# Optimization experiments

Measured on AMD Instinct MI355X. Metric: run time of the kernel, lower is better.

## Reference

```python
import jax, jax.numpy as jnp
import numpy as np

B, S, IN, H, OUT, L = 256, 512, 27, 128, 7, 10


def setup_inputs() -> dict:
    key = jax.random.key(0)
    ks = jax.random.split(key, 12)
    sc = 0.05
    return {
        "x": jax.random.normal(ks[0], (B, S, IN), dtype=jnp.float32),
        # layer 0 input projection (input_size != hidden), PyTorch gate order i,f,g,o
        "w_ih0": jax.random.normal(ks[1], (4 * H, IN), dtype=jnp.float32) * sc,
        # layers 1..9 input projections
        "w_ih": jax.random.normal(ks[2], (L - 1, 4 * H, H), dtype=jnp.float32) * sc,
        "w_hh": jax.random.normal(ks[3], (L, 4 * H, H), dtype=jnp.float32) * sc,
        "b_ih": jax.random.normal(ks[4], (L, 4 * H), dtype=jnp.float32) * sc,
        "b_hh": jax.random.normal(ks[5], (L, 4 * H), dtype=jnp.float32) * sc,
        "attn_w": jax.random.normal(ks[6], (H, H), dtype=jnp.float32) * sc,
        "attn_b": jax.random.normal(ks[7], (H,), dtype=jnp.float32) * sc,
        "v_w": jax.random.normal(ks[8], (1, H), dtype=jnp.float32) * sc,
        "v_b": jax.random.normal(ks[9], (1,), dtype=jnp.float32) * sc,
        "fc_w": jax.random.normal(ks[10], (OUT, H), dtype=jnp.float32) * sc,
        "fc_b": jax.random.normal(ks[11], (OUT,), dtype=jnp.float32) * sc,
    }


def _lstm_layer(x_seq, w_ih, w_hh, b_ih, b_hh):
    # x_seq: [B, S, D_in] -> hidden sequence [B, S, H]
    b, s, _ = x_seq.shape
    h_dim = w_hh.shape[1]
    # precompute input-gate GEMM for the whole sequence (big matmul)
    xg = jnp.einsum('bsd,gd->bsg', x_seq, w_ih) + b_ih + b_hh  # [B, S, 4H]

    def step(carry, xg_t):
        h, c = carry
        gates = xg_t + h @ w_hh.T  # [B, 4H]
        i, f, g, o = jnp.split(gates, 4, axis=-1)
        i = jax.nn.sigmoid(i)
        f = jax.nn.sigmoid(f)
        g = jnp.tanh(g)
        o = jax.nn.sigmoid(o)
        c = f * c + i * g
        h = o * jnp.tanh(c)
        return (h, c), h

    init = (jnp.zeros((b, h_dim), x_seq.dtype), jnp.zeros((b, h_dim), x_seq.dtype))
    _, hs = jax.lax.scan(step, init, jnp.swapaxes(xg, 0, 1))  # [S, B, H]
    return jnp.swapaxes(hs, 0, 1)


def reference(x, w_ih0, w_ih, w_hh, b_ih, b_hh, attn_w, attn_b, v_w, v_b, fc_w, fc_b):
    # 10-layer stacked LSTM (dropout inactive at inference)
    out = _lstm_layer(x, w_ih0, w_hh[0], b_ih[0], b_hh[0])
    for l in range(1, L):
        out = _lstm_layer(out, w_ih[l - 1], w_hh[l], b_ih[l], b_hh[l])
    # additive attention pooling
    scores = jnp.tanh(out @ attn_w.T + attn_b)            # [B, S, H]
    logits = scores @ v_w.T + v_b                          # [B, S, 1]
    weights = jax.nn.softmax(logits, axis=1)               # softmax over time
    context = jnp.sum(weights * out, axis=1)               # [B, H]
    return context @ fc_w.T + fc_b                         # [B, OUT]
```

## Files before the change

### kernel.cpp

```cpp
#include <hip/hip_runtime.h>
#include <cstdint>
#include <cstddef>

#define S_LEN 512
#define HDIM  128
#define G4    512
#define BATCH 256
#define NLAYER 10
#define ROWS  16
#define NBLK  (BATCH / ROWS)
#define RING  10

typedef float f32x4 __attribute__((ext_vector_type(4)));
typedef short short8 __attribute__((ext_vector_type(8)));
typedef _Float16 h16x4 __attribute__((ext_vector_type(4)));
typedef _Float16 h16x8 __attribute__((ext_vector_type(8)));

__device__ __forceinline__ float fsig(float x) {
  return __builtin_amdgcn_rcpf(1.0f + __expf(-x));
}
__device__ __forceinline__ float ftanh(float x) {
  return fmaf(2.0f, __builtin_amdgcn_rcpf(1.0f + __expf(-2.0f * x)), -1.0f);
}
__device__ __forceinline__ unsigned short bf16_rne(float x) {
  unsigned int u = __float_as_uint(x);
  unsigned int r = (u + 0x7fffu + ((u >> 16) & 1u)) >> 16;
  return (unsigned short)r;
}
__device__ __forceinline__ float bf16_to_f(unsigned short h) {
  return __uint_as_float(((unsigned int)h) << 16);
}


__global__ void split_w(const float* __restrict__ W, unsigned short* __restrict__ hi,
                        unsigned short* __restrict__ lo, int n)
{
  int i = blockIdx.x * 256 + threadIdx.x;
  if (i < n) {
    float x = W[i];
    unsigned short h = bf16_rne(x);
    hi[i] = h;
    lo[i] = bf16_rne(x - bf16_to_f(h));
  }
}

__global__ void w0_prep(const float* __restrict__ W, unsigned short* __restrict__ hi,
                        unsigned short* __restrict__ lo)
{
  int i = blockIdx.x * 256 + threadIdx.x;
  if (i >= 512 * 32) return;
  int col = i >> 5, k = i & 31;
  float v = (k < 27) ? W[col * 27 + k] : 0.f;
  unsigned short h = bf16_rne(v);
  hi[i] = h;
  lo[i] = bf16_rne(v - bf16_to_f(h));
}

__global__ __launch_bounds__(256)
void whh_prep(const float* __restrict__ Whh, unsigned short* __restrict__ WF)
{
  int idx = blockIdx.x * 256 + threadIdx.x;
  if (idx >= NLAYER * 16 * 16 * 64) return;
  int ln = idx & 63;
  int f  = (idx >> 6) & 15;
  int w  = (idx >> 10) & 15;
  int l  = idx >> 14;
  int ct = f >> 3, ks = (f >> 1) & 3, hl = f & 1;
  int col = w * 32 + ct * 16 + (ln & 15);
  int k0  = ks * 32 + (ln >> 4) * 8;
  const float* src = Whh + ((size_t)l * G4 + col) * HDIM + k0;
  unsigned short out[8];
  #pragma unroll
  for (int j = 0; j < 8; ++j) {
    float x = src[j];
    unsigned short h = bf16_rne(x);
    out[j] = hl ? bf16_rne(x - bf16_to_f(h)) : h;
  }
  *(short8*)&WF[(size_t)idx * 8] = *(short8*)out;
}

__global__ __launch_bounds__(1024, 4)
void gemm_st(const float* __restrict__ x,
             const float* __restrict__ H0, const float* __restrict__ H1,
             const unsigned short* __restrict__ W0hi, const unsigned short* __restrict__ W0lo,
             const unsigned short* __restrict__ WhiAll, const unsigned short* __restrict__ WloAll,
             const float* __restrict__ bihAll, const float* __restrict__ bhhAll,
             _Float16* __restrict__ XGring, int tchShift, int s, int lmin)
{
  __shared__ unsigned short Ahi[4 * 16 * HDIM];
  __shared__ unsigned short Bhi[64 * HDIM];
  __shared__ unsigned short Blo[64 * HDIM];

  const int l  = lmin + blockIdx.z;
  const int c  = s - l;
  const int bi = blockIdx.x;
  const int tg = blockIdx.y;
  const int tid = threadIdx.x;
  const int t0 = c << tchShift;
  const size_t slotF = ((size_t)BATCH * G4) << tchShift;
  _Float16* __restrict__ XG = XGring + (size_t)(c % RING) * slotF;
  const float* bih = bihAll + l * G4;
  const float* bhh = bhhAll + l * G4;

  {
    int row = tid >> 4;
    int tw = row >> 4, rr = row & 15;
    int ks16 = tid & 15;
    int b = bi * 16 + rr;
    int t = t0 + tg * 4 + tw;
    if (l == 0) {
      if (ks16 < 4) {
        int kg = ks16 * 8;
        const float* ap = &x[((size_t)b * S_LEN + t) * 27];
        unsigned short h8[8];
        #pragma unroll
        for (int j = 0; j < 8; ++j) {
          int k = kg + j;
          float v = (k < 27) ? ap[k] : 0.f;
          h8[j] = bf16_rne(v);
        }
        int byA = tw * 4096 + ((rr * 256 + kg * 2) ^ ((rr & 7) << 4));
        *(short8*)((char*)Ahi + byA) = *(short8*)h8;
      }
    } else {
      int kg = ks16 * 8;
      const float* Asrc = ((l - 1) & 1) ? H1 : H0;
      const float* ap = &Asrc[((size_t)b * S_LEN + t) * HDIM + kg];
      float4 v0 = *(const float4*)ap;
      float4 v1 = *(const float4*)(ap + 4);
      float xs[8] = {v0.x, v0.y, v0.z, v0.w, v1.x, v1.y, v1.z, v1.w};
      unsigned short h8[8];
      #pragma unroll
      for (int j = 0; j < 8; ++j) h8[j] = bf16_rne(xs[j]);
      int byA = tw * 4096 + ((rr * 256 + kg * 2) ^ ((rr & 7) << 4));
      *(short8*)((char*)Ahi + byA) = *(short8*)h8;
    }
  }
  __syncthreads();

  const int ln = tid & 63, lr = ln & 15, lk = ln >> 4;
  const int w16 = tid >> 6;
  const int tw = w16 & 3, cg = w16 >> 2;
  const int tt = tg * 4 + tw;
  const unsigned short* Whi = WhiAll + (size_t)(l - 1) * G4 * HDIM;
  const unsigned short* Wlo = WloAll + (size_t)(l - 1) * G4 * HDIM;

  short8 ah[4];
  #pragma unroll
  for (int ks = 0; ks < 4; ++ks) {
    int fo = (lr * 256 + ks * 64 + lk * 16) ^ ((lr & 7) << 4);
    ah[ks] = *(const short8*)((char*)Ahi + tw * 4096 + fo);
  }
  #pragma unroll
  for (int ks = 0; ks < 4; ++ks) asm("" : "+v"(ah[ks]));

  for (int by = 0; by < 8; ++by) {
    if (l == 0) {
      if (tid < 256) {
        int cc = tid >> 2, kg = (tid & 3) * 8;
        int col = by * 64 + cc;
        int byB = (cc * 256 + kg * 2) ^ ((cc & 7) << 4);
        *(short8*)((char*)Bhi + byB) = *(const short8*)&W0hi[(size_t)col * 32 + kg];
        *(short8*)((char*)Blo + byB) = *(const short8*)&W0lo[(size_t)col * 32 + kg];
      }
    } else {
      int cc = tid >> 4, kg = (tid & 15) * 8;
      int col = by * 64 + cc;
      int byB = (cc * 256 + kg * 2) ^ ((cc & 7) << 4);
      *(short8*)((char*)Bhi + byB) = *(const short8*)&Whi[(size_t)col * HDIM + kg];
      *(short8*)((char*)Blo + byB) = *(const short8*)&Wlo[(size_t)col * HDIM + kg];
    }
    __syncthreads();

    f32x4 acc = {0.f, 0.f, 0.f, 0.f};
    if (l == 0) {
      int fo = (lr * 256 + lk * 16) ^ ((lr & 7) << 4);
      short8 bh = *(const short8*)((char*)Bhi + cg * 4096 + fo);
      short8 bl = *(const short8*)((char*)Blo + cg * 4096 + fo);
      acc = __builtin_amdgcn_mfma_f32_16x16x32_bf16(ah[0], bh, acc, 0, 0, 0);
      acc = __builtin_amdgcn_mfma_f32_16x16x32_bf16(ah[0], bl, acc, 0, 0, 0);
    } else {
      #pragma unroll
      for (int ks = 0; ks < 4; ++ks) {
        int fo = (lr * 256 + ks * 64 + lk * 16) ^ ((lr & 7) << 4);
        short8 bh = *(const short8*)((char*)Bhi + cg * 4096 + fo);
        short8 bl = *(const short8*)((char*)Blo + cg * 4096 + fo);
        acc = __builtin_amdgcn_mfma_f32_16x16x32_bf16(ah[ks], bh, acc, 0, 0, 0);
        acc = __builtin_amdgcn_mfma_f32_16x16x32_bf16(ah[ks], bl, acc, 0, 0, 0);
      }
    }
    int col = by * 64 + cg * 16 + lr;
    float bs = bih[col] + bhh[col];
    h16x4 o;
    #pragma unroll
    for (int j = 0; j < 4; ++j) o[j] = (_Float16)(acc[j] + bs);
    size_t base = ((((size_t)tt * 16 + bi) * 16) + by * 2 + (cg >> 1)) << 9;
    *(h16x4*)(XG + base + ln * 8 + (cg & 1) * 4) = o;
    __syncthreads();
  }
}

__global__ __launch_bounds__(1024, 4)
void scan_mfma(const _Float16* __restrict__ XGring, int tchShift,
               const unsigned short* __restrict__ WF,
               float* __restrict__ H0, float* __restrict__ H1,
               float* __restrict__ cstAll, int s, int lmin)
{
  const int l  = lmin + blockIdx.y;
  const int ch = s - l;
  const int TCHr = 1 << tchShift;
  const int t0 = ch << tchShift;
  const _Float16* __restrict__ XG =
      XGring + (size_t)(ch % RING) * (((size_t)BATCH * G4) << tchShift);
  float* __restrict__ Hout = (l & 1) ? H1 : H0;
  float* __restrict__ cst  = cstAll + (size_t)l * BATCH * HDIM;
  const int B0  = blockIdx.x * ROWS;
  const int tid = threadIdx.x;
  const int w   = tid >> 6;
  const int ln  = tid & 63;
  const int lr  = ln & 15;
  const int lk  = ln >> 4;

  __shared__ unsigned short hA[ROWS * HDIM];
  __shared__ float pp[ROWS * G4];

  short8 bf[16];
  {
    const unsigned short* wfp = WF + (((size_t)l * 16 + w) * 16) * 512 + (size_t)ln * 8;
    #pragma unroll
    for (int f = 0; f < 16; ++f) bf[f] = *(const short8*)(wfp + (size_t)f * 512);
    #pragma unroll
    for (int f = 0; f < 16; ++f) asm("" : "+v"(bf[f]));
  }

  const int grow0 = tid >> 7;
  const int grow1 = grow0 + 8;
  const int ghid  = tid & 127;
  float c0 = 0.f, c1 = 0.f;
  {
    float h0v = 0.f, h1v = 0.f;
    if (t0 > 0) {
      h0v = Hout[((size_t)(B0 + grow0) * S_LEN + (t0 - 1)) * HDIM + ghid];
      h1v = Hout[((size_t)(B0 + grow1) * S_LEN + (t0 - 1)) * HDIM + ghid];
      c0 = cst[(B0 + grow0) * HDIM + ghid];
      c1 = cst[(B0 + grow1) * HDIM + ghid];
    }
    int by0 = (grow0 * 256 + ghid * 2) ^ ((grow0 & 7) << 4);
    int by1 = (grow1 * 256 + ghid * 2) ^ ((grow1 & 7) << 4);
    *(unsigned short*)((char*)hA + by0) = bf16_rne(h0v);
    *(unsigned short*)((char*)hA + by1) = bf16_rne(h1v);
  }
  __syncthreads();

  const _Float16* xgp = XG + (((size_t)blockIdx.x * 16 + w) << 9) + (ln << 3);
  float* hout0 = Hout + ((size_t)(B0 + grow0) * S_LEN + t0) * HDIM + ghid;
  float* hout1 = Hout + ((size_t)(B0 + grow1) * S_LEN + t0) * HDIM + ghid;

  h16x8 xg_c = *(const h16x8*)xgp;

  for (int tt = 0; tt < TCHr; ++tt) {
    const h16x8 xgh = xg_c;
    const _Float16* xgn = xgp + (size_t)BATCH * G4;
    if (tt + 1 < TCHr) xg_c = *(const h16x8*)xgn;

    f32x4 acc0 = {0.f, 0.f, 0.f, 0.f}, acc1 = {0.f, 0.f, 0.f, 0.f};
    #pragma unroll
    for (int ks = 0; ks < 4; ++ks) {
      const int by = (lr * 256 + ks * 64 + lk * 16) ^ ((lr & 7) << 4);
      short8 ah = *(const short8*)((const char*)hA + by);
      acc0 = __builtin_amdgcn_mfma_f32_16x16x32_bf16(ah, bf[(ks << 1) | 0], acc0, 0, 0, 0);
      acc0 = __builtin_amdgcn_mfma_f32_16x16x32_bf16(ah, bf[(ks << 1) | 1], acc0, 0, 0, 0);
      acc1 = __builtin_amdgcn_mfma_f32_16x16x32_bf16(ah, bf[8 | (ks << 1) | 0], acc1, 0, 0, 0);
      acc1 = __builtin_amdgcn_mfma_f32_16x16x32_bf16(ah, bf[8 | (ks << 1) | 1], acc1, 0, 0, 0);
    }

    #pragma unroll
    for (int j = 0; j < 4; ++j) {
      int r16 = lk * 4 + j;
      int colA = w * 32 + lr;
      int byA = (r16 * 2048 + colA * 4) ^ ((r16 & 3) << 5);
      *(float*)((char*)pp + byA) = acc0[j] + (float)xgh[j];
      int colB = colA + 16;
      int byB = (r16 * 2048 + colB * 4) ^ ((r16 & 3) << 5);
      *(float*)((char*)pp + byB) = acc1[j] + (float)xgh[4 + j];
    }
    __syncthreads();

    {
      int b0 = grow0 * 2048, x0 = (grow0 & 3) << 5;
      float pi = *(const float*)((const char*)pp + ((b0 + (ghid)       * 4) ^ x0));
      float pf = *(const float*)((const char*)pp + ((b0 + (128 + ghid) * 4) ^ x0));
      float pg = *(const float*)((const char*)pp + ((b0 + (256 + ghid) * 4) ^ x0));
      float po = *(const float*)((const char*)pp + ((b0 + (384 + ghid) * 4) ^ x0));
      float gi = fsig(pi), gf = fsig(pf), gg = ftanh(pg), go = fsig(po);
      c0 = fmaf(gf, c0, gi * gg);
      float h0 = go * ftanh(c0);

      int b1 = grow1 * 2048, x1 = (grow1 & 3) << 5;
      float qi = *(const float*)((const char*)pp + ((b1 + (ghid)       * 4) ^ x1));
      float qf = *(const float*)((const char*)pp + ((b1 + (128 + ghid) * 4) ^ x1));
      float qg = *(const float*)((const char*)pp + ((b1 + (256 + ghid) * 4) ^ x1));
      float qo = *(const float*)((const char*)pp + ((b1 + (384 + ghid) * 4) ^ x1));
      float hi_ = fsig(qi), hf = fsig(qf), hg = ftanh(qg), ho = fsig(qo);
      c1 = fmaf(hf, c1, hi_ * hg);
      float h1 = ho * ftanh(c1);

      hout0[0] = h0;
      hout1[0] = h1;
      int by0 = (grow0 * 256 + ghid * 2) ^ ((grow0 & 7) << 4);
      int by1 = (grow1 * 256 + ghid * 2) ^ ((grow1 & 7) << 4);
      *(unsigned short*)((char*)hA + by0) = bf16_rne(h0);
      *(unsigned short*)((char*)hA + by1) = bf16_rne(h1);
    }
    __syncthreads();
    xgp = xgn;
    hout0 += HDIM;
    hout1 += HDIM;
  }
  cst[(B0 + grow0) * HDIM + ghid] = c0;
  cst[(B0 + grow1) * HDIM + ghid] = c1;
}

__global__ __launch_bounds__(256, 2)
void attn1_mfma(const float* __restrict__ Hs,
                const unsigned short* __restrict__ AWhi,
                const unsigned short* __restrict__ AWlo,
                const float* __restrict__ attn_b, const float* __restrict__ v_w,
                const float* __restrict__ v_b, float* __restrict__ logits)
{
  __shared__ unsigned short Ahi[64][136];
  __shared__ unsigned short Alo[64][136];
  __shared__ unsigned short Bhi[128][72];
  __shared__ unsigned short Blo[128][72];
  const int tid = threadIdx.x;
  const int rowBase = blockIdx.x * 64;

  #pragma unroll
  for (int it = 0; it < 4; ++it) {
    int idx = tid + it * 256;
    int rr  = idx >> 4;
    int kg  = (idx & 15) * 8;
    const float* ap = &Hs[(size_t)(rowBase + rr) * HDIM + kg];
    float4 v0 = *(const float4*)ap;
    float4 v1 = *(const float4*)(ap + 4);
    float xs[8] = {v0.x, v0.y, v0.z, v0.w, v1.x, v1.y, v1.z, v1.w};
    unsigned short h[8], l8[8];
    #pragma unroll
    for (int j = 0; j < 8; ++j) {
      h[j]  = bf16_rne(xs[j]);
      l8[j] = bf16_rne(xs[j] - bf16_to_f(h[j]));
    }
    *(short8*)&Ahi[rr][kg] = *(short8*)h;
    *(short8*)&Alo[rr][kg] = *(short8*)l8;
  }

  const int w    = tid >> 6;
  const int ln   = tid & 63;
  const int fr   = ln & 15;
  const int kgrp = (ln >> 4) * 8;

  f32x4 acc[8] = {};
  #pragma unroll
  for (int kh = 0; kh < 2; ++kh) {
    __syncthreads();
    #pragma unroll
    for (int it = 0; it < 4; ++it) {
      int idx = tid + it * 256;
      int cc  = idx >> 3;
      int kg  = (idx & 7) * 8;
      *(short8*)&Bhi[cc][kg] = *(const short8*)&AWhi[(size_t)cc * HDIM + kh * 64 + kg];
      *(short8*)&Blo[cc][kg] = *(const short8*)&AWlo[(size_t)cc * HDIM + kh * 64 + kg];
    }
    __syncthreads();
    #pragma unroll
    for (int ks = 0; ks < 2; ++ks) {
      const int k0 = kh * 64 + ks * 32 + kgrp;
      const int kb = ks * 32 + kgrp;
      short8 ah = *(const short8*)&Ahi[(w << 4) + fr][k0];
      short8 al = *(const short8*)&Alo[(w << 4) + fr][k0];
      #pragma unroll
      for (int nt = 0; nt < 8; ++nt) {
        short8 bh = *(const short8*)&Bhi[nt * 16 + fr][kb];
        short8 bl = *(const short8*)&Blo[nt * 16 + fr][kb];
        acc[nt] = __builtin_amdgcn_mfma_f32_16x16x32_bf16(ah, bh, acc[nt], 0, 0, 0);
        acc[nt] = __builtin_amdgcn_mfma_f32_16x16x32_bf16(ah, bl, acc[nt], 0, 0, 0);
        acc[nt] = __builtin_amdgcn_mfma_f32_16x16x32_bf16(al, bh, acc[nt], 0, 0, 0);
      }
    }
  }

  float parts[4] = {0.f, 0.f, 0.f, 0.f};
  #pragma unroll
  for (int nt = 0; nt < 8; ++nt) {
    const int col = nt * 16 + fr;
    const float ab = attn_b[col];
    const float vw = v_w[col];
    #pragma unroll
    for (int j = 0; j < 4; ++j)
      parts[j] = fmaf(ftanh(acc[nt][j] + ab), vw, parts[j]);
  }
  #pragma unroll
  for (int j = 0; j < 4; ++j) {
    #pragma unroll
    for (int off = 1; off < 16; off <<= 1)
      parts[j] += __shfl_xor(parts[j], off);
  }
  if (fr == 0) {
    const float vb = v_b[0];
    #pragma unroll
    for (int j = 0; j < 4; ++j)
      logits[rowBase + (w << 4) + ((ln >> 4) << 2) + j] = parts[j] + vb;
  }
}

__global__ __launch_bounds__(128)
void attn2(const float* __restrict__ Hs, const float* __restrict__ logits,
           const float* __restrict__ fc_w, const float* __restrict__ fc_b,
           float* __restrict__ outp)
{
  const int b   = blockIdx.x;
  const int tid = threadIdx.x;
  __shared__ float pbuf[S_LEN];
  __shared__ float red[4];
  __shared__ float ctx_s[HDIM];
  float l0 = logits[b * S_LEN + tid];
  float l1 = logits[b * S_LEN + 128 + tid];
  float l2 = logits[b * S_LEN + 256 + tid];
  float l3 = logits[b * S_LEN + 384 + tid];
  float m = fmaxf(fmaxf(l0, l1), fmaxf(l2, l3));
  #pragma unroll
  for (int off = 1; off < 64; off <<= 1) m = fmaxf(m, __shfl_xor(m, off));
  if ((tid & 63) == 0) red[tid >> 6] = m;
  __syncthreads();
  m = fmaxf(red[0], red[1]);
  float p0 = __expf(l0 - m), p1 = __expf(l1 - m), p2 = __expf(l2 - m), p3 = __expf(l3 - m);
  pbuf[tid] = p0; pbuf[tid + 128] = p1; pbuf[tid + 256] = p2; pbuf[tid + 384] = p3;
  float sum = (p0 + p1) + (p2 + p3);
  #pragma unroll
  for (int off = 1; off < 64; off <<= 1) sum += __shfl_xor(sum, off);
  if ((tid & 63) == 0) red[2 + (tid >> 6)] = sum;
  __syncthreads();
  const float sinv = 1.0f / (red[2] + red[3]);
  float acc = 0.f;
  const float* hp = Hs + (size_t)b * S_LEN * HDIM + tid;
  #pragma unroll 4
  for (int t = 0; t < S_LEN; ++t) acc = fmaf(pbuf[t], hp[(size_t)t * HDIM], acc);
  ctx_s[tid] = acc * sinv;
  __syncthreads();
  if (tid < 7) {
    float a = fc_b[tid];
    const float* fw = fc_w + tid * HDIM;
    #pragma unroll 8
    for (int k = 0; k < HDIM; ++k) a = fmaf(ctx_s[k], fw[k], a);
    outp[b * 7 + tid] = a;
  }
}

extern "C" void kernel_launch(void* const* d_in, const int* in_sizes, int n_in,
                              void* d_out, int out_size, void* d_ws, size_t ws_size,
                              hipStream_t stream)
{
  const float* x      = (const float*)d_in[0];
  const float* w_ih0  = (const float*)d_in[1];
  const float* w_ih   = (const float*)d_in[2];
  const float* w_hh   = (const float*)d_in[3];
  const float* b_ih   = (const float*)d_in[4];
  const float* b_hh   = (const float*)d_in[5];
  const float* attn_w = (const float*)d_in[6];
  const float* attn_b = (const float*)d_in[7];
  const float* v_w    = (const float*)d_in[8];
  const float* v_b    = (const float*)d_in[9];
  const float* fc_w   = (const float*)d_in[10];
  const float* fc_b   = (const float*)d_in[11];
  float* outp = (float*)d_out;

  const size_t szH_b  = (size_t)BATCH * S_LEN * HDIM * 4;
  const int    nWih   = (NLAYER - 1) * G4 * HDIM;
  const size_t nWF    = (size_t)NLAYER * 16 * 16 * 64 * 8;
  const int    nAW    = HDIM * HDIM;
  const int    nW0    = 512 * 32;
  const size_t fixed  = 2 * szH_b + (size_t)NLAYER * BATCH * HDIM * 4
                      + (size_t)nWih * 2 * 2 + nWF * 2 + (size_t)nAW * 2 * 2
                      + (size_t)nW0 * 2 * 2
                      + (size_t)BATCH * S_LEN * 4;

  int tchShift = -1;
  for (int sh = 6; sh >= 3; --sh) {
    size_t ringBytes = (size_t)RING * (((size_t)BATCH * G4) << sh) * 2;
    if (ws_size >= fixed + ringBytes) { tchShift = sh; break; }
  }
  if (tchShift < 0) return;
  const int TCHr = 1 << tchShift;
  const int NCHr = S_LEN >> tchShift;

  char* p = (char*)d_ws;
  _Float16* XGring = (_Float16*)p;
  p += (size_t)RING * (((size_t)BATCH * G4) << tchShift) * 2;
  float* H0  = (float*)p; p += szH_b;
  float* H1  = (float*)p; p += szH_b;
  float* cst = (float*)p; p += (size_t)NLAYER * BATCH * HDIM * 4;
  float* lg  = (float*)p; p += (size_t)BATCH * S_LEN * 4;
  unsigned short* Whi  = (unsigned short*)p; p += (size_t)nWih * 2;
  unsigned short* Wlo  = (unsigned short*)p; p += (size_t)nWih * 2;
  unsigned short* WF   = (unsigned short*)p; p += nWF * 2;
  unsigned short* AWhi = (unsigned short*)p; p += (size_t)nAW * 2;
  unsigned short* AWlo = (unsigned short*)p; p += (size_t)nAW * 2;
  unsigned short* W0hi = (unsigned short*)p; p += (size_t)nW0 * 2;
  unsigned short* W0lo = (unsigned short*)p; p += (size_t)nW0 * 2;

  split_w<<<(nWih + 255) / 256, 256, 0, stream>>>(w_ih, Whi, Wlo, nWih);
  split_w<<<(nAW + 255) / 256, 256, 0, stream>>>(attn_w, AWhi, AWlo, nAW);
  w0_prep<<<(nW0 + 255) / 256, 256, 0, stream>>>(w_ih0, W0hi, W0lo);
  whh_prep<<<(NLAYER * 16 * 16 * 64 + 255) / 256, 256, 0, stream>>>(w_hh, WF);

  const int TG = TCHr / 4;
  for (int s = 0; s <= NLAYER + NCHr - 2; ++s) {
    int lmin = (s - (NCHr - 1) > 0) ? s - (NCHr - 1) : 0;
    int lmax = (s < NLAYER - 1) ? s : NLAYER - 1;
    int np   = lmax - lmin + 1;
    gemm_st<<<dim3(NBLK, TG, np), 1024, 0, stream>>>(
        x, H0, H1, W0hi, W0lo, Whi, Wlo, b_ih, b_hh, XGring, tchShift, s, lmin);
    scan_mfma<<<dim3(NBLK, np), 1024, 0, stream>>>(
        XGring, tchShift, WF, H0, H1, cst, s, lmin);
  }

  const float* Hlast = H1;
  attn1_mfma<<<dim3(BATCH * S_LEN / 64), 256, 0, stream>>>(
      Hlast, AWhi, AWlo, attn_b, v_w, v_b, lg);
  attn2<<<BATCH, 128, 0, stream>>>(Hlast, lg, fc_w, fc_b, outp);
}
```

Measured before the change: 2.017 ms.

## Permute gate columns so LSTM cell update runs in-register via lane shuffles

Reorders the W_hh fragment columns and the XG output layout so each wave's MFMA accumulators hold all four gates for the same hidden units. The cell update then happens in registers using a lane-xor-8 shuffle, removing the shared-memory gate staging buffer and one barrier per timestep. The h buffer is double-buffered so a single sync per step suffices. In exchange, half of the lanes sit idle during the activation math and the global h stores become less coalesced.

Result: slower. 2.607 ms (+29.3%).

```diff
diff --git a/kernel.cpp b/kernel.cpp
--- a/kernel.cpp
+++ b/kernel.cpp
@@ -66,7 +66,8 @@
   int w  = (idx >> 10) & 15;
   int l  = idx >> 14;
   int ct = f >> 3, ks = (f >> 1) & 3, hl = f & 1;
-  int col = w * 32 + ct * 16 + (ln & 15);
+  int cs  = ct * 16 + (ln & 15);
+  int col = (cs >> 3) * 128 + w * 8 + (cs & 7);
   int k0  = ks * 32 + (ln >> 4) * 8;
   const float* src = Whh + ((size_t)l * G4 + col) * HDIM + k0;
   unsigned short out[8];
@@ -194,8 +195,11 @@
     h16x4 o;
     #pragma unroll
     for (int j = 0; j < 4; ++j) o[j] = (_Float16)(acc[j] + bs);
-    size_t base = ((((size_t)tt * 16 + bi) * 16) + by * 2 + (cg >> 1)) << 9;
-    *(h16x4*)(XG + base + ln * 8 + (cg & 1) * 4) = o;
+    int g    = by >> 1;
+    int slot = ((by & 1) << 3) + (cg << 1) + (lr >> 3);
+    int idx  = (((lk << 4) + ((g & 1) << 3) + (lr & 7)) << 3) + ((g >> 1) << 2);
+    size_t base = ((((size_t)tt * 16 + bi) * 16) + slot) << 9;
+    *(h16x4*)(XG + base + idx) = o;
     __syncthreads();
   }
 }
@@ -221,8 +225,7 @@
   const int lr  = ln & 15;
   const int lk  = ln >> 4;
 
-  __shared__ unsigned short hA[ROWS * HDIM];
-  __shared__ float pp[ROWS * G4];
+  __shared__ unsigned short hA[2][ROWS * HDIM];
 
   short8 bf[16];
   {
@@ -233,28 +236,28 @@
     for (int f = 0; f < 16; ++f) asm("" : "+v"(bf[f]));
   }
 
-  const int grow0 = tid >> 7;
-  const int grow1 = grow0 + 8;
-  const int ghid  = tid & 127;
-  float c0 = 0.f, c1 = 0.f;
+  const int hid  = (w << 3) + (lr & 7);
+  const bool low = (lr & 8) == 0;
+  float c4[4] = {0.f, 0.f, 0.f, 0.f};
   {
-    float h0v = 0.f, h1v = 0.f;
-    if (t0 > 0) {
-      h0v = Hout[((size_t)(B0 + grow0) * S_LEN + (t0 - 1)) * HDIM + ghid];
-      h1v = Hout[((size_t)(B0 + grow1) * S_LEN + (t0 - 1)) * HDIM + ghid];
-      c0 = cst[(B0 + grow0) * HDIM + ghid];
-      c1 = cst[(B0 + grow1) * HDIM + ghid];
-    }
-    int by0 = (grow0 * 256 + ghid * 2) ^ ((grow0 & 7) << 4);
-    int by1 = (grow1 * 256 + ghid * 2) ^ ((grow1 & 7) << 4);
-    *(unsigned short*)((char*)hA + by0) = bf16_rne(h0v);
-    *(unsigned short*)((char*)hA + by1) = bf16_rne(h1v);
+    #pragma unroll
+    for (int j = 0; j < 4; ++j) {
+      int row = (lk << 2) + j;
+      float hv = 0.f;
+      if (t0 > 0) {
+        hv    = Hout[((size_t)(B0 + row) * S_LEN + (t0 - 1)) * HDIM + hid];
+        c4[j] = cst[(B0 + row) * HDIM + hid];
+      }
+      if (low) {
+        int byh = (row * 256 + hid * 2) ^ ((row & 7) << 4);
+        *(unsigned short*)((char*)hA[0] + byh) = bf16_rne(hv);
+      }
+    }
   }
   __syncthreads();
 
   const _Float16* xgp = XG + (((size_t)blockIdx.x * 16 + w) << 9) + (ln << 3);
-  float* hout0 = Hout + ((size_t)(B0 + grow0) * S_LEN + t0) * HDIM + ghid;
-  float* hout1 = Hout + ((size_t)(B0 + grow1) * S_LEN + t0) * HDIM + ghid;
+  float* houtB = Hout + ((size_t)(B0 + (lk << 2)) * S_LEN + t0) * HDIM + hid;
 
   h16x8 xg_c = *(const h16x8*)xgp;
 
@@ -263,62 +266,57 @@
     const _Float16* xgn = xgp + (size_t)BATCH * G4;
     if (tt + 1 < TCHr) xg_c = *(const h16x8*)xgn;
 
+    const unsigned short* hAr = hA[tt & 1];
     f32x4 acc0 = {0.f, 0.f, 0.f, 0.f}, acc1 = {0.f, 0.f, 0.f, 0.f};
     #pragma unroll
     for (int ks = 0; ks < 4; ++ks) {
       const int by = (lr * 256 + ks * 64 + lk * 16) ^ ((lr & 7) << 4);
-      short8 ah = *(const short8*)((const char*)hA + by);
-      acc0 = __builtin_amdgcn_mfma_f32_16x16x32_bf16(ah, bf[(ks << 1) | 0], acc0, 0, 0, 0);
-      acc0 = __builtin_amdgcn_mfma_f32_16x16x32_bf16(ah, bf[(ks << 1) | 1], acc0, 0, 0, 0);
-      acc1 = __builtin_amdgcn_mfma_f32_16x16x32_bf16(ah, bf[8 | (ks << 1) | 0], acc1, 0, 0, 0);
-      acc1 = __builtin_amdgcn_mfma_f32_16x16x32_bf16(ah, bf[8 | (ks << 1) | 1], acc1, 0, 0, 0);
-    }
-
+      short8 ahf = *(const short8*)((const char*)hAr + by);
+      acc0 = __builtin_amdgcn_mfma_f32_16x16x32_bf16(ahf, bf[(ks << 1) | 0], acc0, 0, 0, 0);
+      acc0 = __builtin_amdgcn_mfma_f32_16x16x32_bf16(ahf, bf[(ks << 1) | 1], acc0, 0, 0, 0);
+      acc1 = __builtin_amdgcn_mfma_f32_16x16x32_bf16(ahf, bf[8 | (ks << 1) | 0], acc1, 0, 0, 0);
+      acc1 = __builtin_amdgcn_mfma_f32_16x16x32_bf16(ahf, bf[8 | (ks << 1) | 1], acc1, 0, 0, 0);
+    }
+
+    float p0[4], p1[4], q0[4], q1[4];
     #pragma unroll
     for (int j = 0; j < 4; ++j) {
-      int r16 = lk * 4 + j;
-      int colA = w * 32 + lr;
-      int byA = (r16 * 2048 + colA * 4) ^ ((r16 & 3) << 5);
-      *(float*)((char*)pp + byA) = acc0[j] + (float)xgh[j];
-      int colB = colA + 16;
-      int byB = (r16 * 2048 + colB * 4) ^ ((r16 & 3) << 5);
-      *(float*)((char*)pp + byB) = acc1[j] + (float)xgh[4 + j];
-    }
-    __syncthreads();
-
-    {
-      int b0 = grow0 * 2048, x0 = (grow0 & 3) << 5;
-      float pi = *(const float*)((const char*)pp + ((b0 + (ghid)       * 4) ^ x0));
-      float pf = *(const float*)((const char*)pp + ((b0 + (128 + ghid) * 4) ^ x0));
-      float pg = *(const float*)((const char*)pp + ((b0 + (256 + ghid) * 4) ^ x0));
-      float po = *(const float*)((const char*)pp + ((b0 + (384 + ghid) * 4) ^ x0));
-      float gi = fsig(pi), gf = fsig(pf), gg = ftanh(pg), go = fsig(po);
-      c0 = fmaf(gf, c0, gi * gg);
-      float h0 = go * ftanh(c0);
-
-      int b1 = grow1 * 2048, x1 = (grow1 & 3) << 5;
-      float qi = *(const float*)((const char*)pp + ((b1 + (ghid)       * 4) ^ x1));
-      float qf = *(const float*)((const char*)pp + ((b1 + (128 + ghid) * 4) ^ x1));
-      float qg = *(const float*)((const char*)pp + ((b1 + (256 + ghid) * 4) ^ x1));
-      float qo = *(const float*)((const char*)pp + ((b1 + (384 + ghid) * 4) ^ x1));
-      float hi_ = fsig(qi), hf = fsig(qf), hg = ftanh(qg), ho = fsig(qo);
-      c1 = fmaf(hf, c1, hi_ * hg);
-      float h1 = ho * ftanh(c1);
-
-      hout0[0] = h0;
-      hout1[0] = h1;
-      int by0 = (grow0 * 256 + ghid * 2) ^ ((grow0 & 7) << 4);
-      int by1 = (grow1 * 256 + ghid * 2) ^ ((grow1 & 7) << 4);
-      *(unsigned short*)((char*)hA + by0) = bf16_rne(h0);
-      *(unsigned short*)((char*)hA + by1) = bf16_rne(h1);
+      p0[j] = acc0[j] + (float)xgh[j];
+      p1[j] = acc1[j] + (float)xgh[4 + j];
+    }
+    #pragma unroll
+    for (int j = 0; j < 4; ++j) {
+      q0[j] = __shfl_xor(p0[j], 8);
+      q1[j] = __shfl_xor(p1[j], 8);
+    }
+
+    unsigned short* hAw = hA[(tt & 1) ^ 1];
+    #pragma unroll
+    for (int j = 0; j < 4; ++j) {
+      float pi_ = low ? p0[j] : q0[j];
+      float pf_ = low ? q0[j] : p0[j];
+      float pg_ = low ? p1[j] : q1[j];
+      float po_ = low ? q1[j] : p1[j];
+      float gi = fsig(pi_), gf = fsig(pf_);
+      float gg = ftanh(pg_), go = fsig(po_);
+      c4[j] = fmaf(gf, c4[j], gi * gg);
+      float h = go * ftanh(c4[j]);
+      if (low) {
+        houtB[(size_t)j * S_LEN * HDIM] = h;
+        int row = (lk << 2) + j;
+        int byh = (row * 256 + hid * 2) ^ ((row & 7) << 4);
+        *(unsigned short*)((char*)hAw + byh) = bf16_rne(h);
+      }
     }
     __syncthreads();
     xgp = xgn;
-    hout0 += HDIM;
-    hout1 += HDIM;
-  }
-  cst[(B0 + grow0) * HDIM + ghid] = c0;
-  cst[(B0 + grow1) * HDIM + ghid] = c1;
+    houtB += HDIM;
+  }
+  if (low) {
+    #pragma unroll
+    for (int j = 0; j < 4; ++j)
+      cst[(B0 + (lk << 2) + j) * HDIM + hid] = c4[j];
+  }
 }
 
 __global__ __launch_bounds__(256, 2)
```
